# Kernel optimization log

Hardware: AMD Instinct MI355X
Metric: run time of the kernel (lower is better)

Reference implementation:

```python
import jax, jax.numpy as jnp
import numpy as np
import math

N, C, T, V = 32, 64, 400, 27
S = 2            # num_subset
IC = 16          # inter_channels
EPS = 1e-5


def _spatial_pe(channels, num_node):
    # PositionalEncoding(domain='spatial'): pe[c, t, v] depends only on joint id v
    pos = jnp.arange(num_node, dtype=jnp.float32)                      # [V]
    div = jnp.exp(jnp.arange(0, channels, 2, dtype=jnp.float32)
                  * (-math.log(10000.0) / channels))                   # [C/2]
    ang = div[:, None] * pos[None, :]                                  # [C/2, V]
    pe = jnp.stack([jnp.sin(ang), jnp.cos(ang)], axis=1)               # [C/2, 2, V]
    return pe.reshape(channels, num_node)                              # [C, V]


def _conv1x1(x, w, b):
    # x: [N, Cin, T, V], w: [Cout, Cin]
    return jnp.einsum('nctv,oc->notv', x, w) + b[None, :, None, None]


def _bn(x, g, b, m, v):
    inv = g / jnp.sqrt(v + EPS)
    return x * inv[None, :, None, None] + (b - m * inv)[None, :, None, None]


def _leaky(x):
    return jnp.where(x >= 0, x, 0.1 * x)


def setup_inputs() -> dict:
    key = jax.random.key(0)
    ks = jax.random.split(key, 24)
    d = {}
    d['x'] = jax.random.normal(ks[0], (N, C, T, V), jnp.float32)
    d['w_in'] = jax.random.normal(ks[1], (2 * S * IC, C), jnp.float32) * 0.1
    d['b_in'] = jax.random.normal(ks[2], (2 * S * IC,), jnp.float32) * 0.05
    d['alphas'] = jnp.ones((1, S, 1, 1), jnp.float32)
    d['att0'] = jax.random.uniform(ks[3], (1, S, V, V), jnp.float32) / V
    d['w_outs'] = jax.random.normal(ks[4], (C, S * C), jnp.float32) * 0.08
    d['b_outs'] = jax.random.normal(ks[5], (C,), jnp.float32) * 0.05
    d['bn_outs_g'] = jax.random.uniform(ks[6], (C,), jnp.float32) + 0.5
    d['bn_outs_b'] = jax.random.normal(ks[7], (C,), jnp.float32) * 0.05
    d['bn_outs_m'] = jax.random.normal(ks[8], (C,), jnp.float32) * 0.1
    d['bn_outs_v'] = jax.random.uniform(ks[9], (C,), jnp.float32) + 0.5
    d['w_ff'] = jax.random.normal(ks[10], (C, C), jnp.float32) * 0.1
    d['b_ff'] = jax.random.normal(ks[11], (C,), jnp.float32) * 0.05
    d['bn_ff_g'] = jax.random.uniform(ks[12], (C,), jnp.float32) + 0.5
    d['bn_ff_b'] = jax.random.normal(ks[13], (C,), jnp.float32) * 0.05
    d['bn_ff_m'] = jax.random.normal(ks[14], (C,), jnp.float32) * 0.1
    d['bn_ff_v'] = jax.random.uniform(ks[15], (C,), jnp.float32) + 0.5
    d['w_t'] = jax.random.normal(ks[16], (C, C, 3, 1), jnp.float32) * 0.08
    d['b_t'] = jax.random.normal(ks[17], (C,), jnp.float32) * 0.05
    d['bn_t_g'] = jax.random.uniform(ks[18], (C,), jnp.float32) + 0.5
    d['bn_t_b'] = jax.random.normal(ks[19], (C,), jnp.float32) * 0.05
    d['bn_t_m'] = jax.random.normal(ks[20], (C,), jnp.float32) * 0.1
    d['bn_t_v'] = jax.random.uniform(ks[21], (C,), jnp.float32) + 0.5
    return d


def reference(x, w_in, b_in, alphas, att0,
              w_outs, b_outs, bn_outs_g, bn_outs_b, bn_outs_m, bn_outs_v,
              w_ff, b_ff, bn_ff_g, bn_ff_b, bn_ff_m, bn_ff_v,
              w_t, b_t, bn_t_g, bn_t_b, bn_t_m, bn_t_v):
    n, c, t, v = x.shape
    # spatial positional encoding (broadcast over T)
    pe = _spatial_pe(c, v)                                      # [C, V]
    y = x + pe[None, :, None, :]
    # q/k projection: 1x1 conv -> [N, 2S, IC, T, V], chunk on subset axis
    qk = _conv1x1(y, w_in, b_in).reshape(n, 2 * S, IC, t, v)
    q, k = qk[:, :S], qk[:, S:]
    # tanh attention over joints + learnable global bias (atts buffer is zeros)
    att = jnp.tanh(jnp.einsum('nsctu,nsctv->nsuv', q, k) / (IC * t)) * alphas
    att = att + att0                                            # [N, S, V, V]
    # aggregate V-dim: [N, S, C, T, V] -> [N, S*C, T, V]
    y = jnp.einsum('nctu,nsuv->nsctv', x, att).reshape(n, S * c, t, v)
    y = _bn(_conv1x1(y, w_outs, b_outs), bn_outs_g, bn_outs_b, bn_outs_m, bn_outs_v)
    y = _leaky(x + y)                                           # downs1 = identity
    y2 = _bn(_conv1x1(y, w_ff, b_ff), bn_ff_g, bn_ff_b, bn_ff_m, bn_ff_v)
    y2 = _leaky(x + y2)                                         # downs2 = identity
    # temporal conv (3,1), padding (1,0), stride 1
    z = jax.lax.conv_general_dilated(
        y2, w_t, window_strides=(1, 1), padding=((1, 1), (0, 0)),
        dimension_numbers=('NCHW', 'OIHW', 'NCHW')) + b_t[None, :, None, None]
    z = _bn(z, bn_t_g, bn_t_b, bn_t_m, bn_t_v)
    z = _leaky(y2 + z)                                          # downt2 = identity
    return z
```

## Files before the change

kernel.cpp:

```cpp
#include <hip/hip_runtime.h>
#include <hip/hip_bf16.h>
#include <math.h>


typedef __hip_bfloat16 bf16;
typedef unsigned short u16t;
typedef unsigned int u32t;

using bf16x8 = __attribute__((ext_vector_type(8))) short;
using f32x4  = __attribute__((ext_vector_type(4))) float;

#define NN 32
#define CH 64
#define TT 400
#define VV 27
#define PIX 10800
#define NSUV (32*2*27*27)
#define XTOT (NN*CH*PIX)

#define TB1 4
#define NT1 100
#define TB2 4
#define NT2 100
#define TBS 9
#define NTS 45

__device__ __forceinline__ float lrelu(float x) { return x >= 0.f ? x : 0.1f * x; }
__device__ __forceinline__ float4 ld4(const float* p) { return *reinterpret_cast<const float4*>(p); }
__device__ __forceinline__ uint2 ld2u(const u32t* p) { return *reinterpret_cast<const uint2*>(p); }

__device__ __forceinline__ u16t f2bf(float f) {
    return __bfloat16_as_ushort(__float2bfloat16(f));
}
__device__ __forceinline__ u32t packbf(float lo, float hi) {
    return ((u32t)f2bf(hi) << 16) | (u32t)f2bf(lo);
}
__device__ __forceinline__ float bf2f(u16t u) {
    return __uint_as_float(((u32t)u) << 16);
}
__device__ __forceinline__ u32t cvtpk(float lo, float hi) {
    u32t r;
    asm("v_cvt_pk_bf16_f32 %0, %1, %2" : "=v"(r) : "v"(lo), "v"(hi));
    return r;
}
__device__ __forceinline__ void dot2v(float& c, u32t a, u32t b) {
    asm("v_dot2_f32_bf16 %0, %1, %2, %0" : "+v"(c) : "v"(a), "v"(b));
}
__device__ __forceinline__ void dot2s(float& c, u32t a_sgpr, u32t b) {
    asm("v_dot2_f32_bf16 %0, %1, %2, %0" : "+v"(c) : "s"(a_sgpr), "v"(b));
}

__global__ void k_prep(
    const float* __restrict__ w_outs, const float* __restrict__ b_outs,
    const float* __restrict__ go, const float* __restrict__ bo,
    const float* __restrict__ mo, const float* __restrict__ vo,
    const float* __restrict__ w_ff, const float* __restrict__ b_ff,
    const float* __restrict__ gf, const float* __restrict__ bf,
    const float* __restrict__ mf, const float* __restrict__ vf,
    const float* __restrict__ w_t, const float* __restrict__ b_t,
    const float* __restrict__ gt, const float* __restrict__ btb,
    const float* __restrict__ mt, const float* __restrict__ vt,
    const float* __restrict__ w_in,
    u16t* __restrict__ wfoA, float* __restrict__ bfo,
    u16t* __restrict__ wffA, float* __restrict__ bff,
    u16t* __restrict__ wtA, float* __restrict__ bft,
    u32t* __restrict__ wqkpk)
{
    const int total = 8192 + 4096 + 12288 + 192 + 2048;
    for (int idx = blockIdx.x * 256 + threadIdx.x; idx < total; idx += gridDim.x * 256) {
        if (idx < 8192) {
            int o = idx >> 7, j = idx & 127;
            float inv = go[o] * rsqrtf(vo[o] + 1e-5f);
            wfoA[idx] = f2bf(w_outs[o * 128 + j] * inv);
        } else if (idx < 12288) {
            int r = idx - 8192; int o = r >> 6, c = r & 63;
            float inv = gf[o] * rsqrtf(vf[o] + 1e-5f);
            wffA[r] = f2bf(w_ff[o * 64 + c] * inv);
        } else if (idx < 24576) {
            int r = idx - 12288;
            int o = r / 192, k2 = r % 192;
            int kt = k2 >> 6, c = k2 & 63;
            float inv = gt[o] * rsqrtf(vt[o] + 1e-5f);
            wtA[r] = f2bf(w_t[o * 192 + c * 3 + kt] * inv);
        } else if (idx < 24768) {
            int r = idx - 24576; int o = r & 63, which = r >> 6;
            if (which == 0) {
                float inv = go[o] * rsqrtf(vo[o] + 1e-5f);
                bfo[o] = b_outs[o] * inv + bo[o] - mo[o] * inv;
            } else if (which == 1) {
                float inv = gf[o] * rsqrtf(vf[o] + 1e-5f);
                bff[o] = b_ff[o] * inv + bf[o] - mf[o] * inv;
            } else {
                float inv = gt[o] * rsqrtf(vt[o] + 1e-5f);
                bft[o] = b_t[o] * inv + btb[o] - mt[o] * inv;
            }
        } else {
            int i = idx - 24768;
            int cc2 = i & 31, c = (i >> 5) & 15, sq = i >> 9;
            int s = sq >> 1, qk = sq & 1;
            int row = qk * 32 + s * 16 + c;
            wqkpk[i] = packbf(w_in[row * 64 + 2 * cc2], w_in[row * 64 + 2 * cc2 + 1]);
        }
    }
}

__global__ __launch_bounds__(256) void k_pbias(
    const float* __restrict__ w_in, const float* __restrict__ b_in,
    float* __restrict__ pb)
{
    __shared__ float pe[64 * 27];
    const int tid = threadIdx.x;
    for (int idx = tid; idx < 1728; idx += 256) {
        int c = idx / 27, u = idx % 27;
        float div = expf(-0.28782313662425575f * (float)(c >> 1));
        float ang = div * (float)u;
        pe[idx] = (c & 1) ? cosf(ang) : sinf(ang);
    }
    __syncthreads();
    for (int idx = tid; idx < 1792; idx += 256) {
        int u = idx % 28, r = idx / 28;
        int c = r % 16, sq = r / 16;
        if (u >= 27) { pb[idx] = 0.f; continue; }
        int s = sq >> 1, qk = sq & 1;
        int row = qk * 32 + s * 16 + c;
        float acc = b_in[row];
        for (int cc = 0; cc < 64; ++cc) acc += w_in[row * 64 + cc] * pe[cc * 27 + u];
        pb[idx] = acc;
    }
}

__global__ __launch_bounds__(256, 4) void k_scores(
    const float* __restrict__ x, const u32t* __restrict__ wqkpk,
    const float* __restrict__ pb, float* __restrict__ scores)
{
    const int tid = threadIdx.x;
    const int s = blockIdx.y, n = blockIdx.z;
    const int t0 = blockIdx.x * TBS;

    __shared__ u32t qlds[TBS * 27 * 10];
    __shared__ u32t klds[TBS * 27 * 10];

    const int pcl = tid < 243 ? tid : 242;
    const int tt = pcl / 27, u = pcl - tt * 27;
    const int t = t0 + tt;
    const bool valid = (tid < 243) && (t < TT);

    u32t xp[32];
    const float* xb = x + (size_t)n * 64 * PIX + (size_t)(t < TT ? t : 0) * 27 + u;
    #pragma unroll
    for (int c2 = 0; c2 < 32; ++c2) {
        float v0 = xb[(size_t)(2 * c2) * PIX];
        float v1 = xb[(size_t)(2 * c2 + 1) * PIX];
        xp[c2] = cvtpk(v0, v1);
    }

    const float* pbq = pb + ((s * 2 + 0) * 16) * 28 + u;
    const float* pbk = pb + ((s * 2 + 1) * 16) * 28 + u;
    const u32t* wq = wqkpk + (s * 2 + 0) * 16 * 32;
    const u32t* wk = wqkpk + (s * 2 + 1) * 16 * 32;
    float qr[16], kr[16];
    #pragma unroll
    for (int c = 0; c < 16; ++c) { qr[c] = pbq[c * 28]; kr[c] = pbk[c * 28]; }
    #pragma unroll
    for (int c = 0; c < 16; ++c) {
        const u32t* wr = wq + c * 32;
        #pragma unroll
        for (int c2 = 0; c2 < 32; ++c2) dot2s(qr[c], wr[c2], xp[c2]);
    }
    #pragma unroll
    for (int c = 0; c < 16; ++c) {
        const u32t* wr = wk + c * 32;
        #pragma unroll
        for (int c2 = 0; c2 < 32; ++c2) dot2s(kr[c], wr[c2], xp[c2]);
    }

    if (tid < 243) {
        #pragma unroll
        for (int c2 = 0; c2 < 8; ++c2) {
            qlds[(tt * 27 + u) * 10 + c2] = valid ? cvtpk(qr[2 * c2], qr[2 * c2 + 1]) : 0u;
            klds[(tt * 27 + u) * 10 + c2] = valid ? cvtpk(kr[2 * c2], kr[2 * c2 + 1]) : 0u;
        }
    }
    __syncthreads();

    const int sid = tid < 243 ? tid : 242;
    const int ug = sid / 9, vg = sid % 9;
    const int v0 = vg * 3;
    float sc0 = 0.f, sc1 = 0.f, sc2 = 0.f;
    for (int t2 = 0; t2 < TBS; ++t2) {
        const u32t* qrow = qlds + (t2 * 27 + ug) * 10;
        const u32t* k0 = klds + (t2 * 27 + v0) * 10;
        #pragma unroll
        for (int c4 = 0; c4 < 4; ++c4) {
            uint2 qp = ld2u(qrow + c4 * 2);
            uint2 ka = ld2u(k0 + c4 * 2);
            uint2 kb = ld2u(k0 + 10 + c4 * 2);
            uint2 kc = ld2u(k0 + 20 + c4 * 2);
            dot2v(sc0, qp.x, ka.x); dot2v(sc0, qp.y, ka.y);
            dot2v(sc1, qp.x, kb.x); dot2v(sc1, qp.y, kb.y);
            dot2v(sc2, qp.x, kc.x); dot2v(sc2, qp.y, kc.y);
        }
    }
    if (tid < 243) {
        float* sb = scores + (n * 2 + s) * 729 + ug * 27 + v0;
        atomicAdd(&sb[0], sc0);
        atomicAdd(&sb[1], sc1);
        atomicAdd(&sb[2], sc2);
    }
}

__global__ void k_att(const float* __restrict__ scores,
                      const float* __restrict__ alphas,
                      const float* __restrict__ att0,
                      u32t* __restrict__ attTp)
{
    int i = blockIdx.x * 256 + threadIdx.x;
    if (i >= NN * 2 * 32 * 16) return;
    int e = i & 15;
    int r = i >> 4;
    int v = r & 31;
    int ns = r >> 5;
    int s = ns & 1;
    if (v >= 27) { attTp[i] = 0u; return; }
    const float* sb = scores + ns * 729;
    const float* ab = att0 + s * 729;
    float al = alphas[s];
    int u0 = 2 * e, u1 = 2 * e + 1;
    float a0 = (u0 < 27) ? tanhf(sb[u0 * 27 + v] * (1.f / 6400.f)) * al + ab[u0 * 27 + v] : 0.f;
    float a1 = (u1 < 27) ? tanhf(sb[u1 * 27 + v] * (1.f / 6400.f)) * al + ab[u1 * 27 + v] : 0.f;
    attTp[i] = packbf(a0, a1);
}

__global__ __launch_bounds__(256, 2) void k_stage1(
    const float* __restrict__ x, const u32t* __restrict__ attTp,
    const u16t* __restrict__ wfoA, const float* __restrict__ bfo,
    const u16t* __restrict__ wffA, const float* __restrict__ bff,
    u16t* __restrict__ y2)
{
    const int tid = threadIdx.x;
    const int n = blockIdx.y, t0 = blockIdx.x * TB1;
    const int w = tid >> 6, li = tid & 15, g = (tid >> 4) & 3;

    __shared__ __align__(16) u16t xs[64 * TB1 * 32];
    __shared__ __align__(16) u32t mmL[112 * 68];
    __shared__ __align__(16) u32t y1L[112 * 34];

    for (int i = tid; i < 8192; i += 256) {
        int u = i & 31, ct = i >> 5;
        int tt = ct & 3, c = ct >> 2;
        float val = (u < 27) ? x[(size_t)(n * 64 + c) * PIX + (t0 + tt) * 27 + u] : 0.f;
        xs[i] = f2bf(val);
    }
    for (int i = tid; i < 112 * 68; i += 256) mmL[i] = 0u;
    for (int i = tid; i < 112 * 34; i += 256) y1L[i] = 0u;
    __syncthreads();

    {
        bf16x8 ax[4];
        #pragma unroll
        for (int Mt = 0; Mt < 4; ++Mt)
            ax[Mt] = *reinterpret_cast<const bf16x8*>(&xs[((Mt * 16 + li) * 4 + w) * 32 + g * 8]);
        const u16t* attp16 = reinterpret_cast<const u16t*>(attTp);
        #pragma unroll
        for (int s = 0; s < 2; ++s) {
            #pragma unroll
            for (int Nt = 0; Nt < 2; ++Nt) {
                bf16x8 b = *reinterpret_cast<const bf16x8*>(
                    &attp16[(((n * 2 + s) * 32) + Nt * 16 + li) * 32 + g * 8]);
                const int v = Nt * 16 + li;
                #pragma unroll
                for (int Mt = 0; Mt < 4; ++Mt) {
                    f32x4 d = {0.f, 0.f, 0.f, 0.f};
                    d = __builtin_amdgcn_mfma_f32_16x16x32_bf16(ax[Mt], b, d, 0, 0, 0);
                    if (v < 28) {
                        const int p = w * 28 + v;
                        const int j2 = s * 32 + Mt * 8 + g * 2;
                        mmL[p * 68 + j2]     = packbf(d[0], d[1]);
                        mmL[p * 68 + j2 + 1] = packbf(d[2], d[3]);
                    }
                }
            }
        }
    }
    __syncthreads();

    const int o0 = w * 16 + g * 4;
    {
        bf16x8 aw[4];
        #pragma unroll
        for (int Ks = 0; Ks < 4; ++Ks)
            aw[Ks] = *reinterpret_cast<const bf16x8*>(&wfoA[(w * 16 + li) * 128 + Ks * 32 + g * 8]);
        float4 bf4 = ld4(&bfo[o0]);
        #pragma unroll
        for (int Nt = 0; Nt < 7; ++Nt) {
            f32x4 d = {0.f, 0.f, 0.f, 0.f};
            #pragma unroll
            for (int Ks = 0; Ks < 4; ++Ks) {
                bf16x8 b = *reinterpret_cast<const bf16x8*>(&mmL[(Nt * 16 + li) * 68 + Ks * 16 + g * 4]);
                d = __builtin_amdgcn_mfma_f32_16x16x32_bf16(aw[Ks], b, d, 0, 0, 0);
            }
            const int p = Nt * 16 + li;
            const int tt = p / 28, v = p - tt * 28;
            float ya = lrelu(bf2f(xs[((o0 + 0) * 4 + tt) * 32 + v]) + d[0] + bf4.x);
            float yb = lrelu(bf2f(xs[((o0 + 1) * 4 + tt) * 32 + v]) + d[1] + bf4.y);
            float yc = lrelu(bf2f(xs[((o0 + 2) * 4 + tt) * 32 + v]) + d[2] + bf4.z);
            float yd = lrelu(bf2f(xs[((o0 + 3) * 4 + tt) * 32 + v]) + d[3] + bf4.w);
            y1L[p * 34 + w * 8 + g * 2]     = packbf(ya, yb);
            y1L[p * 34 + w * 8 + g * 2 + 1] = packbf(yc, yd);
        }
    }
    __syncthreads();

    {
        bf16x8 af[2];
        #pragma unroll
        for (int Ks = 0; Ks < 2; ++Ks)
            af[Ks] = *reinterpret_cast<const bf16x8*>(&wffA[(w * 16 + li) * 64 + Ks * 32 + g * 8]);
        float4 bff4 = ld4(&bff[o0]);
        #pragma unroll
        for (int Nt = 0; Nt < 7; ++Nt) {
            f32x4 d = {0.f, 0.f, 0.f, 0.f};
            #pragma unroll
            for (int Ks = 0; Ks < 2; ++Ks) {
                union { uint2 u2[2]; bf16x8 v8; } bu;
                bu.u2[0] = *reinterpret_cast<const uint2*>(&y1L[(Nt * 16 + li) * 34 + Ks * 16 + g * 4]);
                bu.u2[1] = *reinterpret_cast<const uint2*>(&y1L[(Nt * 16 + li) * 34 + Ks * 16 + g * 4 + 2]);
                d = __builtin_amdgcn_mfma_f32_16x16x32_bf16(af[Ks], bu.v8, d, 0, 0, 0);
            }
            const int p = Nt * 16 + li;
            const int tt = p / 28, v = p - tt * 28;
            if (v < 27) {
                u16t* yb0 = y2 + (size_t)(n * 64) * PIX + (size_t)(t0 + tt) * 27 + v;
                yb0[(size_t)(o0 + 0) * PIX] = f2bf(lrelu(bf2f(xs[((o0 + 0) * 4 + tt) * 32 + v]) + d[0] + bff4.x));
                yb0[(size_t)(o0 + 1) * PIX] = f2bf(lrelu(bf2f(xs[((o0 + 1) * 4 + tt) * 32 + v]) + d[1] + bff4.y));
                yb0[(size_t)(o0 + 2) * PIX] = f2bf(lrelu(bf2f(xs[((o0 + 2) * 4 + tt) * 32 + v]) + d[2] + bff4.z));
                yb0[(size_t)(o0 + 3) * PIX] = f2bf(lrelu(bf2f(xs[((o0 + 3) * 4 + tt) * 32 + v]) + d[3] + bff4.w));
            }
        }
    }
}

__global__ __launch_bounds__(256, 4) void k_stage2(
    const u16t* __restrict__ y2in, const u16t* __restrict__ wtA,
    const float* __restrict__ bft, float* __restrict__ out)
{
    const int tid = threadIdx.x;
    const int n = blockIdx.y, t0 = blockIdx.x * TB2;
    const int w = tid >> 6, li = tid & 15, g = (tid >> 4) & 3;

    __shared__ __align__(16) u16t ys[6 * 28 * 72];

    for (int idx = tid; idx < 6 * 28 * 64; idx += 256) {
        int v = idx % 28, r = idx / 28;
        int tp = r % 6, c = r / 6;
        int t = t0 - 1 + tp;
        ys[(tp * 28 + v) * 72 + c] = (v < 27 && t >= 0 && t < TT)
            ? y2in[(size_t)(n * 64 + c) * PIX + t * 27 + v] : (u16t)0;
    }
    __syncthreads();

    const int o0 = w * 16 + g * 4;
    bf16x8 aw[6];
    #pragma unroll
    for (int Ks = 0; Ks < 6; ++Ks)
        aw[Ks] = *reinterpret_cast<const bf16x8*>(&wtA[(w * 16 + li) * 192 + Ks * 32 + g * 8]);
    float4 bt4 = ld4(&bft[o0]);

    #pragma unroll
    for (int Nt = 0; Nt < 7; ++Nt) {
        const int p = Nt * 16 + li;
        const int tt = p / 28, v = p - tt * 28;
        f32x4 d = {0.f, 0.f, 0.f, 0.f};
        #pragma unroll
        for (int Ks = 0; Ks < 6; ++Ks) {
            const int kt = Ks >> 1, c0 = (Ks & 1) * 32 + g * 8;
            bf16x8 b = *reinterpret_cast<const bf16x8*>(&ys[((tt + kt) * 28 + v) * 72 + c0]);
            d = __builtin_amdgcn_mfma_f32_16x16x32_bf16(aw[Ks], b, d, 0, 0, 0);
        }
        if (v < 27) {
            float* ob = out + (size_t)(n * 64) * PIX + (size_t)(t0 + tt) * 27 + v;
            float r0 = bf2f(ys[((tt + 1) * 28 + v) * 72 + o0 + 0]);
            float r1 = bf2f(ys[((tt + 1) * 28 + v) * 72 + o0 + 1]);
            float r2 = bf2f(ys[((tt + 1) * 28 + v) * 72 + o0 + 2]);
            float r3 = bf2f(ys[((tt + 1) * 28 + v) * 72 + o0 + 3]);
            ob[(size_t)(o0 + 0) * PIX] = lrelu(r0 + d[0] + bt4.x);
            ob[(size_t)(o0 + 1) * PIX] = lrelu(r1 + d[1] + bt4.y);
            ob[(size_t)(o0 + 2) * PIX] = lrelu(r2 + d[2] + bt4.z);
            ob[(size_t)(o0 + 3) * PIX] = lrelu(r3 + d[3] + bt4.w);
        }
    }
}

extern "C" void kernel_launch(void* const* d_in, const int* in_sizes, int n_in,
                              void* d_out, int out_size, void* d_ws, size_t ws_size,
                              hipStream_t stream)
{
    const float* x      = (const float*)d_in[0];
    const float* w_in   = (const float*)d_in[1];
    const float* b_in   = (const float*)d_in[2];
    const float* alphas = (const float*)d_in[3];
    const float* att0   = (const float*)d_in[4];
    const float* w_outs = (const float*)d_in[5];
    const float* b_outs = (const float*)d_in[6];
    const float* bog    = (const float*)d_in[7];
    const float* bob    = (const float*)d_in[8];
    const float* bom    = (const float*)d_in[9];
    const float* bov    = (const float*)d_in[10];
    const float* w_ff   = (const float*)d_in[11];
    const float* b_ff   = (const float*)d_in[12];
    const float* bfg    = (const float*)d_in[13];
    const float* bfb    = (const float*)d_in[14];
    const float* bfm    = (const float*)d_in[15];
    const float* bfv    = (const float*)d_in[16];
    const float* w_t    = (const float*)d_in[17];
    const float* b_t    = (const float*)d_in[18];
    const float* btg    = (const float*)d_in[19];
    const float* btb    = (const float*)d_in[20];
    const float* btm    = (const float*)d_in[21];
    const float* btv    = (const float*)d_in[22];

    float* pbw    = (float*)d_ws;
    float* scores = pbw + 1792;
    u32t*  attTp  = (u32t*)(scores + NSUV);
    u16t*  wfoA   = (u16t*)(attTp + 32768);
    u16t*  wffA   = (u16t*)((u32t*)wfoA + 4096);
    u16t*  wtA    = (u16t*)((u32t*)wffA + 2048);
    float* bfo    = (float*)((u32t*)wtA + 6144);
    float* bff    = bfo + 64;
    float* bft    = bff + 64;
    u32t*  wqkpk  = (u32t*)(bft + 64);
    u16t*  y2     = (u16t*)(wqkpk + 2048);

    hipMemsetAsync(scores, 0, NSUV * sizeof(float), stream);

    k_prep<<<32, 256, 0, stream>>>(w_outs, b_outs, bog, bob, bom, bov,
                                   w_ff, b_ff, bfg, bfb, bfm, bfv,
                                   w_t, b_t, btg, btb, btm, btv, w_in,
                                   wfoA, bfo, wffA, bff, wtA, bft, wqkpk);
    k_pbias<<<1, 256, 0, stream>>>(w_in, b_in, pbw);
    k_scores<<<dim3(NTS, 2, NN), 256, 0, stream>>>(x, wqkpk, pbw, scores);
    k_att<<<(NN * 2 * 32 * 16 + 255) / 256, 256, 0, stream>>>(scores, alphas, att0, attTp);
    k_stage1<<<dim3(NT1, NN), 256, 0, stream>>>(x, attTp, wfoA, bfo, wffA, bff, y2);
    k_stage2<<<dim3(NT2, NN), 256, 0, stream>>>(y2, wtA, bft, (float*)d_out);
}
```

Baseline: 421.0 us.

## Double stage1 block to 512 threads, swizzle x tile, drop LDS zero-init

k_stage1 now runs 512 threads per block. Each wave handles one (time, subset) pair in the attention GEMM, and each half of the block takes half of the N tiles in the two channel-mixing GEMMs. The x tile moves to a time-major layout with an XOR swizzle and is loaded two elements at a time packed into u32, which should cut LDS bank conflicts on the MFMA operand reads. The zero-fill of the mmL and y1L scratch buffers is removed, since every location that is read is also written. The tighter launch bounds (512, 4) limit registers per thread and may cause spills.

```diff
diff --git a/kernel.cpp b/kernel.cpp
--- a/kernel.cpp
+++ b/kernel.cpp
@@ -231,7 +231,7 @@
     attTp[i] = packbf(a0, a1);
 }
 
-__global__ __launch_bounds__(256, 2) void k_stage1(
+__global__ __launch_bounds__(512, 4) void k_stage1(
     const float* __restrict__ x, const u32t* __restrict__ attTp,
     const u16t* __restrict__ wfoA, const float* __restrict__ bfo,
     const u16t* __restrict__ wffA, const float* __restrict__ bff,
@@ -241,58 +241,64 @@
     const int n = blockIdx.y, t0 = blockIdx.x * TB1;
     const int w = tid >> 6, li = tid & 15, g = (tid >> 4) & 3;
 
-    __shared__ __align__(16) u16t xs[64 * TB1 * 32];
+    __shared__ __align__(16) u16t xs[4 * 64 * 32];
     __shared__ __align__(16) u32t mmL[112 * 68];
     __shared__ __align__(16) u32t y1L[112 * 34];
 
-    for (int i = tid; i < 8192; i += 256) {
-        int u = i & 31, ct = i >> 5;
-        int tt = ct & 3, c = ct >> 2;
-        float val = (u < 27) ? x[(size_t)(n * 64 + c) * PIX + (t0 + tt) * 27 + u] : 0.f;
-        xs[i] = f2bf(val);
-    }
-    for (int i = tid; i < 112 * 68; i += 256) mmL[i] = 0u;
-    for (int i = tid; i < 112 * 34; i += 256) y1L[i] = 0u;
+    for (int j = tid; j < 4096; j += 512) {
+        int i = j & 15, c = (j >> 4) & 63, tt = j >> 10;
+        const float* xrow = x + (size_t)(n * 64 + c) * PIX + (size_t)(t0 + tt) * 27;
+        int u0 = 2 * i;
+        float v0 = (u0 < 27) ? xrow[u0] : 0.f;
+        float v1 = (u0 + 1 < 27) ? xrow[u0 + 1] : 0.f;
+        int ip = i ^ (((c >> 1) & 3) << 2);
+        reinterpret_cast<u32t*>(xs)[(tt * 64 + c) * 16 + ip] = packbf(v0, v1);
+    }
     __syncthreads();
 
     {
+        const int t = w & 3, s = w >> 2;
         bf16x8 ax[4];
         #pragma unroll
-        for (int Mt = 0; Mt < 4; ++Mt)
-            ax[Mt] = *reinterpret_cast<const bf16x8*>(&xs[((Mt * 16 + li) * 4 + w) * 32 + g * 8]);
+        for (int Mt = 0; Mt < 4; ++Mt) {
+            const int c = Mt * 16 + li;
+            const int blk = g ^ ((li >> 1) & 3);
+            ax[Mt] = *reinterpret_cast<const bf16x8*>(&xs[(t * 64 + c) * 32 + blk * 8]);
+        }
         const u16t* attp16 = reinterpret_cast<const u16t*>(attTp);
         #pragma unroll
-        for (int s = 0; s < 2; ++s) {
+        for (int Nt = 0; Nt < 2; ++Nt) {
+            bf16x8 b = *reinterpret_cast<const bf16x8*>(
+                &attp16[(((n * 2 + s) * 32) + Nt * 16 + li) * 32 + g * 8]);
+            const int v = Nt * 16 + li;
             #pragma unroll
-            for (int Nt = 0; Nt < 2; ++Nt) {
-                bf16x8 b = *reinterpret_cast<const bf16x8*>(
-                    &attp16[(((n * 2 + s) * 32) + Nt * 16 + li) * 32 + g * 8]);
-                const int v = Nt * 16 + li;
-                #pragma unroll
-                for (int Mt = 0; Mt < 4; ++Mt) {
-                    f32x4 d = {0.f, 0.f, 0.f, 0.f};
-                    d = __builtin_amdgcn_mfma_f32_16x16x32_bf16(ax[Mt], b, d, 0, 0, 0);
-                    if (v < 28) {
-                        const int p = w * 28 + v;
-                        const int j2 = s * 32 + Mt * 8 + g * 2;
-                        mmL[p * 68 + j2]     = packbf(d[0], d[1]);
-                        mmL[p * 68 + j2 + 1] = packbf(d[2], d[3]);
-                    }
+            for (int Mt = 0; Mt < 4; ++Mt) {
+                f32x4 d = {0.f, 0.f, 0.f, 0.f};
+                d = __builtin_amdgcn_mfma_f32_16x16x32_bf16(ax[Mt], b, d, 0, 0, 0);
+                if (v < 28) {
+                    const int p = t * 28 + v;
+                    const int j2 = s * 32 + Mt * 8 + g * 2;
+                    mmL[p * 68 + j2]     = packbf(d[0], d[1]);
+                    mmL[p * 68 + j2 + 1] = packbf(d[2], d[3]);
                 }
             }
         }
     }
     __syncthreads();
 
-    const int o0 = w * 16 + g * 4;
+    const int ot = w & 3, hh = w >> 2;
+    const int o0 = ot * 16 + g * 4;
+
     {
         bf16x8 aw[4];
         #pragma unroll
         for (int Ks = 0; Ks < 4; ++Ks)
-            aw[Ks] = *reinterpret_cast<const bf16x8*>(&wfoA[(w * 16 + li) * 128 + Ks * 32 + g * 8]);
+            aw[Ks] = *reinterpret_cast<const bf16x8*>(&wfoA[(ot * 16 + li) * 128 + Ks * 32 + g * 8]);
         float4 bf4 = ld4(&bfo[o0]);
         #pragma unroll
-        for (int Nt = 0; Nt < 7; ++Nt) {
+        for (int q = 0; q < 4; ++q) {
+            const int Nt = hh * 4 + q;
+            if (Nt >= 7) continue;
             f32x4 d = {0.f, 0.f, 0.f, 0.f};
             #pragma unroll
             for (int Ks = 0; Ks < 4; ++Ks) {
@@ -301,12 +307,14 @@
             }
             const int p = Nt * 16 + li;
             const int tt = p / 28, v = p - tt * 28;
-            float ya = lrelu(bf2f(xs[((o0 + 0) * 4 + tt) * 32 + v]) + d[0] + bf4.x);
-            float yb = lrelu(bf2f(xs[((o0 + 1) * 4 + tt) * 32 + v]) + d[1] + bf4.y);
-            float yc = lrelu(bf2f(xs[((o0 + 2) * 4 + tt) * 32 + v]) + d[2] + bf4.z);
-            float yd = lrelu(bf2f(xs[((o0 + 3) * 4 + tt) * 32 + v]) + d[3] + bf4.w);
-            y1L[p * 34 + w * 8 + g * 2]     = packbf(ya, yb);
-            y1L[p * 34 + w * 8 + g * 2 + 1] = packbf(yc, yd);
+            const int sw0 = ((o0 >> 1) & 3) << 3;
+            const int sw1 = (((o0 + 2) >> 1) & 3) << 3;
+            float ya = lrelu(bf2f(xs[(tt * 64 + o0 + 0) * 32 + (v ^ sw0)]) + d[0] + bf4.x);
+            float yb = lrelu(bf2f(xs[(tt * 64 + o0 + 1) * 32 + (v ^ sw0)]) + d[1] + bf4.y);
+            float yc = lrelu(bf2f(xs[(tt * 64 + o0 + 2) * 32 + (v ^ sw1)]) + d[2] + bf4.z);
+            float yd = lrelu(bf2f(xs[(tt * 64 + o0 + 3) * 32 + (v ^ sw1)]) + d[3] + bf4.w);
+            y1L[p * 34 + ot * 8 + g * 2]     = packbf(ya, yb);
+            y1L[p * 34 + ot * 8 + g * 2 + 1] = packbf(yc, yd);
         }
     }
     __syncthreads();
@@ -315,10 +323,12 @@
         bf16x8 af[2];
         #pragma unroll
         for (int Ks = 0; Ks < 2; ++Ks)
-            af[Ks] = *reinterpret_cast<const bf16x8*>(&wffA[(w * 16 + li) * 64 + Ks * 32 + g * 8]);
+            af[Ks] = *reinterpret_cast<const bf16x8*>(&wffA[(ot * 16 + li) * 64 + Ks * 32 + g * 8]);
         float4 bff4 = ld4(&bff[o0]);
         #pragma unroll
-        for (int Nt = 0; Nt < 7; ++Nt) {
+        for (int q = 0; q < 4; ++q) {
+            const int Nt = hh * 4 + q;
+            if (Nt >= 7) continue;
             f32x4 d = {0.f, 0.f, 0.f, 0.f};
             #pragma unroll
             for (int Ks = 0; Ks < 2; ++Ks) {
@@ -330,11 +340,13 @@
             const int p = Nt * 16 + li;
             const int tt = p / 28, v = p - tt * 28;
             if (v < 27) {
+                const int sw0 = ((o0 >> 1) & 3) << 3;
+                const int sw1 = (((o0 + 2) >> 1) & 3) << 3;
                 u16t* yb0 = y2 + (size_t)(n * 64) * PIX + (size_t)(t0 + tt) * 27 + v;
-                yb0[(size_t)(o0 + 0) * PIX] = f2bf(lrelu(bf2f(xs[((o0 + 0) * 4 + tt) * 32 + v]) + d[0] + bff4.x));
-                yb0[(size_t)(o0 + 1) * PIX] = f2bf(lrelu(bf2f(xs[((o0 + 1) * 4 + tt) * 32 + v]) + d[1] + bff4.y));
-                yb0[(size_t)(o0 + 2) * PIX] = f2bf(lrelu(bf2f(xs[((o0 + 2) * 4 + tt) * 32 + v]) + d[2] + bff4.z));
-                yb0[(size_t)(o0 + 3) * PIX] = f2bf(lrelu(bf2f(xs[((o0 + 3) * 4 + tt) * 32 + v]) + d[3] + bff4.w));
+                yb0[(size_t)(o0 + 0) * PIX] = f2bf(lrelu(bf2f(xs[(tt * 64 + o0 + 0) * 32 + (v ^ sw0)]) + d[0] + bff4.x));
+                yb0[(size_t)(o0 + 1) * PIX] = f2bf(lrelu(bf2f(xs[(tt * 64 + o0 + 1) * 32 + (v ^ sw0)]) + d[1] + bff4.y));
+                yb0[(size_t)(o0 + 2) * PIX] = f2bf(lrelu(bf2f(xs[(tt * 64 + o0 + 2) * 32 + (v ^ sw1)]) + d[2] + bff4.z));
+                yb0[(size_t)(o0 + 3) * PIX] = f2bf(lrelu(bf2f(xs[(tt * 64 + o0 + 3) * 32 + (v ^ sw1)]) + d[3] + bff4.w));
             }
         }
     }
@@ -440,6 +452,6 @@
     k_pbias<<<1, 256, 0, stream>>>(w_in, b_in, pbw);
     k_scores<<<dim3(NTS, 2, NN), 256, 0, stream>>>(x, wqkpk, pbw, scores);
     k_att<<<(NN * 2 * 32 * 16 + 255) / 256, 256, 0, stream>>>(scores, alphas, att0, attTp);
-    k_stage1<<<dim3(NT1, NN), 256, 0, stream>>>(x, attTp, wfoA, bfo, wffA, bff, y2);
+    k_stage1<<<dim3(NT1, NN), 512, 0, stream>>>(x, attTp, wfoA, bfo, wffA, bff, y2);
     k_stage2<<<dim3(NT2, NN), 256, 0, stream>>>(y2, wtA, bft, (float*)d_out);
 }
```

Result: faster. 383.0 us (-9.0%).
